# Performance work log

Measured on AMD Instinct MI355X. Metric: run time of the kernel, lower is better.

The kernel has to match this reference:

```python
import jax, jax.numpy as jnp
import numpy as np
import math

DIM = 1024
HEADS = 16
HEAD_DIM = DIM // HEADS
ROT = min(HEAD_DIM, 32)  # rotary_dim
B, S = 2, 1024


def setup_inputs() -> dict:
    key = jax.random.key(0)
    ks = jax.random.split(key, 32)
    lin = lambda k: jax.random.normal(k, (DIM, DIM), jnp.float32) * 0.02
    bias = lambda k: jax.random.normal(k, (DIM,), jnp.float32) * 0.01
    inp = {
        'real': jax.random.normal(ks[0], (B, S, DIM), jnp.float32),
        'imag': jax.random.normal(ks[1], (B, S, DIM), jnp.float32),
        'Wq_r': lin(ks[2]), 'bq_r': bias(ks[3]),
        'Wk_r': lin(ks[4]), 'bk_r': bias(ks[5]),
        'Wv_r': lin(ks[6]), 'bv_r': bias(ks[7]),
        'Wq_i': lin(ks[8]), 'bq_i': bias(ks[9]),
        'Wk_i': lin(ks[10]), 'bk_i': bias(ks[11]),
        'Wv_i': lin(ks[12]), 'bv_i': bias(ks[13]),
        'Wo_r': lin(ks[14]), 'bo_r': bias(ks[15]),
        'Wo_i': lin(ks[16]), 'bo_i': bias(ks[17]),
        'phase_shifts': jax.random.normal(ks[18], (HEADS, HEAD_DIM), jnp.float32) * 0.02,
        'ent': jnp.eye(HEADS, dtype=jnp.float32) + jax.random.normal(ks[19], (HEADS, HEADS), jnp.float32) * 0.01,
        'rot_freqs': (10000.0 ** (-jnp.arange(0, ROT, 2, dtype=jnp.float32) / ROT)),
        'strength': jnp.ones((1,), jnp.float32),
        'temp': jnp.ones((1,), jnp.float32),
    }
    return inp


def _fwd(real, imag, Wq_r, bq_r, Wk_r, bk_r, Wv_r, bv_r,
         Wq_i, bq_i, Wk_i, bk_i, Wv_i, bv_i,
         Wo_r, bo_r, Wo_i, bo_i,
         phase_shifts, ent, rot_freqs, strength, temp):
    b, s, _ = real.shape
    to_heads = lambda t: t.reshape(b, s, HEADS, HEAD_DIM).transpose(0, 2, 1, 3)  # bhsd
    lin = lambda x, W, bb: x @ W + bb

    q_r = to_heads(lin(real, Wq_r, bq_r))
    k_r = to_heads(lin(real, Wk_r, bk_r))
    v_r = to_heads(lin(real, Wv_r, bv_r))
    q_i = to_heads(lin(imag, Wq_i, bq_i))
    k_i = to_heads(lin(imag, Wk_i, bk_i))
    v_i = to_heads(lin(imag, Wv_i, bv_i))

    # rotary on first ROT dims (pairwise rotation)
    pos = jnp.arange(s, dtype=jnp.float32)
    emb = pos[:, None] * rot_freqs[None, :]           # [S, ROT/2]
    cos = jnp.cos(emb)[None, None]                    # [1,1,S,ROT/2]
    sin = jnp.sin(emb)[None, None]

    def rope(t):
        tr = t[..., :ROT].reshape(b, HEADS, s, ROT // 2, 2)
        r0 = tr[..., 0] * cos - tr[..., 1] * sin
        r1 = tr[..., 1] * cos + tr[..., 0] * sin
        rr = jnp.stack([r0, r1], axis=-1).reshape(b, HEADS, s, ROT)
        return jnp.concatenate([rr, t[..., ROT:]], axis=-1)

    q_r, k_r = rope(q_r), rope(k_r)
    q_i, k_i = rope(q_i), rope(k_i)

    # entanglement mixing across heads
    mix = lambda t: jnp.einsum('bhsd,hx->bxsd', t, ent)
    q_r, q_i, k_r, k_i = mix(q_r), mix(q_i), mix(k_r), mix(k_i)

    # per-head phase shift (complex rotation)
    pc = jnp.cos(phase_shifts)[None, :, None, :]      # [1,H,1,D]
    ps = jnp.sin(phase_shifts)[None, :, None, :]
    q_r, q_i = q_r * pc - q_i * ps, q_r * ps + q_i * pc
    k_r, k_i = k_r * pc - k_i * ps, k_r * ps + k_i * pc

    scale = 1.0 / math.sqrt(HEAD_DIM)
    attn_r = (jnp.einsum('bhqd,bhkd->bhqk', q_r, k_r) + jnp.einsum('bhqd,bhkd->bhqk', q_i, k_i)) * scale
    attn_i = (jnp.einsum('bhqd,bhkd->bhqk', q_i, k_r) - jnp.einsum('bhqd,bhkd->bhqk', q_r, k_i)) * scale
    attn_mag = jnp.sqrt(attn_r ** 2 + attn_i ** 2 + 1e-6)

    causal = jnp.triu(jnp.ones((s, s), dtype=bool), k=1)[None, None]
    attn_mag = jnp.where(causal, -jnp.inf, attn_mag)

    t = jnp.maximum(temp, 0.01)
    g = jax.nn.sigmoid(strength)
    attn = jax.nn.softmax(attn_mag * g / t, axis=-1)

    out_r = jnp.einsum('bhqk,bhkd->bhqd', attn, v_r).transpose(0, 2, 1, 3).reshape(b, s, DIM)
    out_i = jnp.einsum('bhqk,bhkd->bhqd', attn, v_i).transpose(0, 2, 1, 3).reshape(b, s, DIM)
    return lin(out_r, Wo_r, bo_r), lin(out_i, Wo_i, bo_i)


def reference(real, imag, Wq_r, bq_r, Wk_r, bk_r, Wv_r, bv_r,
              Wq_i, bq_i, Wk_i, bk_i, Wv_i, bv_i,
              Wo_r, bo_r, Wo_i, bo_i,
              phase_shifts, ent, rot_freqs, strength, temp):
    return _fwd(real, imag, Wq_r, bq_r, Wk_r, bk_r, Wv_r, bv_r,
                Wq_i, bq_i, Wk_i, bk_i, Wv_i, bv_i,
                Wo_r, bo_r, Wo_i, bo_i,
                phase_shifts, ent, rot_freqs, strength, temp)
```

## Files before the change

### kernel.cpp

```cpp
#include <hip/hip_runtime.h>
#include <stdint.h>

typedef unsigned short u16;
typedef __bf16 bf16x8 __attribute__((ext_vector_type(8)));
typedef float f32x4 __attribute__((ext_vector_type(4)));
typedef unsigned int u32x4 __attribute__((ext_vector_type(4)));

__device__ __forceinline__ u16 f2bf(float f) {
  uint32_t u = __float_as_uint(f);
  u += 0x7FFFu + ((u >> 16) & 1u);
  return (u16)(u >> 16);
}
__device__ __forceinline__ float bf2f(u16 h) {
  return __uint_as_float(((uint32_t)h) << 16);
}
__device__ __forceinline__ void gld16(const void* g, void* lds) {
  __builtin_amdgcn_global_load_lds(
      (const __attribute__((address_space(1))) uint32_t*)g,
      (__attribute__((address_space(3))) uint32_t*)lds, 16, 0, 0);
}
__device__ __forceinline__ f32x4 mfma16(u32x4 a, u32x4 b, f32x4 c) {
  return __builtin_amdgcn_mfma_f32_16x16x32_bf16(
      __builtin_bit_cast(bf16x8, a), __builtin_bit_cast(bf16x8, b), c, 0, 0, 0);
}

__global__ __launch_bounds__(256) void convx_kernel(const float* __restrict__ real,
                                                    const float* __restrict__ imag,
                                                    u16* __restrict__ Xr,
                                                    u16* __restrict__ Xi) {
  int u = blockIdx.x * 256 + threadIdx.x;
  int a = u >> 18;
  int r = u & 262143;
  int m = r >> 7, slot = r & 127;
  const float* src = (a ? imag : real) + (size_t)m * 1024 + slot * 8;
  int slot2 = (slot & ~7) | ((slot ^ m) & 7);
  u16* dst = (a ? Xi : Xr) + (size_t)m * 1024 + slot2 * 8;
  f32x4 v0 = *(const f32x4*)(src);
  f32x4 v1 = *(const f32x4*)(src + 4);
  union { u16 h[8]; u32x4 v; } o;
#pragma unroll
  for (int e = 0; e < 4; ++e) { o.h[e] = f2bf(v0[e]); o.h[4 + e] = f2bf(v1[e]); }
  *(u32x4*)dst = o.v;
}

__global__ __launch_bounds__(256) void convw_kernel(
    const float* __restrict__ w0, const float* __restrict__ w1,
    const float* __restrict__ w2, const float* __restrict__ w3,
    const float* __restrict__ w4, const float* __restrict__ w5,
    const float* __restrict__ w6, const float* __restrict__ w7,
    u16* __restrict__ WtAll) {
  __shared__ float Lt[64][65];
  int z = blockIdx.z;
  const float* W = (z == 0) ? w0 : (z == 1) ? w1 : (z == 2) ? w2 : (z == 3) ? w3
                 : (z == 4) ? w4 : (z == 5) ? w5 : (z == 6) ? w6 : w7;
  u16* Wt = WtAll + (size_t)z * (1024 * 1024);
  int tid = threadIdx.x;
  int n0 = blockIdx.x * 64, k0 = blockIdx.y * 64;
#pragma unroll
  for (int it = 0; it < 4; ++it) {
    int idx = it * 256 + tid;
    int kr = idx >> 4, nc = (idx & 15) * 4;
    f32x4 v = *(const f32x4*)(W + (size_t)(k0 + kr) * 1024 + n0 + nc);
#pragma unroll
    for (int e = 0; e < 4; ++e) Lt[kr][nc + e] = v[e];
  }
  __syncthreads();
#pragma unroll
  for (int it = 0; it < 2; ++it) {
    int idx = it * 256 + tid;
    int nr = idx >> 3, sl = idx & 7;
    union { u16 h[8]; u32x4 v; } o;
#pragma unroll
    for (int e = 0; e < 8; ++e) o.h[e] = f2bf(Lt[sl * 8 + e][nr]);
    int sl2 = sl ^ (nr & 7);
    *(u32x4*)(Wt + (size_t)(n0 + nr) * 1024 + k0 + sl2 * 8) = o.v;
  }
}

__device__ __forceinline__ void gemm128(const u16* __restrict__ A, const u16* __restrict__ W,
                                        const float* __restrict__ bias,
                                        u16* __restrict__ outB, float* __restrict__ outF) {
  __shared__ __align__(16) u16 As[128 * 64];
  __shared__ __align__(16) u16 Bs[128 * 64];
  int tid = threadIdx.x, l = tid & 63, w = tid >> 6;
  int lr = l & 15, lh = l >> 4;
  int m0 = blockIdx.y * 128, n0 = blockIdx.x * 128;
  int wr = w >> 1, wc = w & 1;
  f32x4 acc[4][4];
#pragma unroll
  for (int mi = 0; mi < 4; ++mi)
#pragma unroll
    for (int ni = 0; ni < 4; ++ni) acc[mi][ni] = f32x4{0.f, 0.f, 0.f, 0.f};

  for (int kt = 0; kt < 16; ++kt) {
#pragma unroll
    for (int c = 0; c < 4; ++c) {
      int chunk = c * 4 + w;
      int i = chunk * 64 + l;
      int row = i >> 3, off = i & 7;
      gld16(A + (size_t)(m0 + row) * 1024 + kt * 64 + off * 8, (char*)As + chunk * 1024);
      gld16(W + (size_t)(n0 + row) * 1024 + kt * 64 + off * 8, (char*)Bs + chunk * 1024);
    }
    __syncthreads();
#pragma unroll
    for (int kk = 0; kk < 2; ++kk) {
      u32x4 af[4], bf[4];
#pragma unroll
      for (int mi = 0; mi < 4; ++mi) {
        int row = wr * 64 + mi * 16 + lr;
        af[mi] = *(const u32x4*)((const char*)As + row * 128 +
                                 ((kk * 64 + lh * 16) ^ ((row & 7) << 4)));
      }
#pragma unroll
      for (int ni = 0; ni < 4; ++ni) {
        int row = wc * 64 + ni * 16 + lr;
        bf[ni] = *(const u32x4*)((const char*)Bs + row * 128 +
                                 ((kk * 64 + lh * 16) ^ ((row & 7) << 4)));
      }
#pragma unroll
      for (int mi = 0; mi < 4; ++mi)
#pragma unroll
        for (int ni = 0; ni < 4; ++ni)
          acc[mi][ni] = mfma16(af[mi], bf[ni], acc[mi][ni]);
    }
    __syncthreads();
  }
#pragma unroll
  for (int ni = 0; ni < 4; ++ni) {
    int col = n0 + wc * 64 + ni * 16 + lr;
    float bv = bias[col];
#pragma unroll
    for (int mi = 0; mi < 4; ++mi)
#pragma unroll
      for (int rr = 0; rr < 4; ++rr) {
        int row = m0 + wr * 64 + mi * 16 + 4 * lh + rr;
        float v = acc[mi][ni][rr] + bv;
        if (outF) outF[(size_t)row * 1024 + col] = v;
        else      outB[(size_t)row * 1024 + col] = f2bf(v);
      }
  }
}

__global__ __launch_bounds__(256) void gemm_proj_kernel(
    const u16* __restrict__ Xr, const u16* __restrict__ Xi, const u16* __restrict__ Wt,
    const float* b0, const float* b1, const float* b2,
    const float* b3, const float* b4, const float* b5,
    u16* __restrict__ qkv) {
  int z = blockIdx.z;
  const u16* A = (z < 3) ? Xr : Xi;
  const u16* W = Wt + (size_t)z * (1024 * 1024);
  const float* bias = (z == 0) ? b0 : (z == 1) ? b1 : (z == 2) ? b2
                    : (z == 3) ? b3 : (z == 4) ? b4 : b5;
  u16* out = qkv + (size_t)z * (2048 * 1024);
  gemm128(A, W, bias, out, nullptr);
}

__global__ __launch_bounds__(256) void gemm_out_kernel(
    const u16* __restrict__ O, const u16* __restrict__ Wt2,
    const float* br, const float* bi, float* __restrict__ dout) {
  int z = blockIdx.z;
  gemm128(O + (size_t)z * (2048 * 1024), Wt2 + (size_t)z * (1024 * 1024),
          z ? bi : br, nullptr, dout + (size_t)z * (2048 * 1024));
}

__global__ __launch_bounds__(256) void transform_kernel(
    const u16* __restrict__ qkv, const float* __restrict__ phase,
    const float* __restrict__ ent, const float* __restrict__ rotf,
    u16* __restrict__ Qr, u16* __restrict__ Qi, u16* __restrict__ Kr,
    u16* __restrict__ Ki, u16* __restrict__ Vr, u16* __restrict__ Vi) {
  __shared__ float Lqr[16][65], Lqi[16][65], Lkr[16][65], Lki[16][65];
  __shared__ float sent[256];
  int tid = threadIdx.x;
  int bs = blockIdx.x;
  int b = bs >> 10, s = bs & 1023;
  sent[tid] = ent[tid];
  const u16* qr_raw = qkv;
  const u16* kr_raw = qkv + (size_t)1 * 2048 * 1024;
  const u16* vr_raw = qkv + (size_t)2 * 2048 * 1024;
  const u16* qi_raw = qkv + (size_t)3 * 2048 * 1024;
  const u16* ki_raw = qkv + (size_t)4 * 2048 * 1024;
  const u16* vi_raw = qkv + (size_t)5 * 2048 * 1024;
  size_t rowoff = (size_t)bs * 1024;
#pragma unroll
  for (int it = 0; it < 2; ++it) {
    int u = it * 256 + tid;
    int hh = u >> 5, j = u & 31;
    int base = hh * 64 + 2 * j;
    uint32_t aqr = *(const uint32_t*)(qr_raw + rowoff + base);
    uint32_t aqi = *(const uint32_t*)(qi_raw + rowoff + base);
    uint32_t akr = *(const uint32_t*)(kr_raw + rowoff + base);
    uint32_t aki = *(const uint32_t*)(ki_raw + rowoff + base);
    float qr0 = bf2f((u16)aqr), qr1 = bf2f((u16)(aqr >> 16));
    float qi0 = bf2f((u16)aqi), qi1 = bf2f((u16)(aqi >> 16));
    float kr0 = bf2f((u16)akr), kr1 = bf2f((u16)(akr >> 16));
    float ki0 = bf2f((u16)aki), ki1 = bf2f((u16)(aki >> 16));
    if (j < 16) {
      float sn, cs;
      sincosf((float)s * rotf[j], &sn, &cs);
      float t0;
      t0 = qr0; qr0 = t0 * cs - qr1 * sn; qr1 = qr1 * cs + t0 * sn;
      t0 = qi0; qi0 = t0 * cs - qi1 * sn; qi1 = qi1 * cs + t0 * sn;
      t0 = kr0; kr0 = t0 * cs - kr1 * sn; kr1 = kr1 * cs + t0 * sn;
      t0 = ki0; ki0 = t0 * cs - ki1 * sn; ki1 = ki1 * cs + t0 * sn;
    }
    int d0 = 2 * j;
    Lqr[hh][d0] = qr0; Lqr[hh][d0 + 1] = qr1;
    Lqi[hh][d0] = qi0; Lqi[hh][d0 + 1] = qi1;
    Lkr[hh][d0] = kr0; Lkr[hh][d0 + 1] = kr1;
    Lki[hh][d0] = ki0; Lki[hh][d0 + 1] = ki1;
  }
  __syncthreads();
#pragma unroll
  for (int it = 0; it < 4; ++it) {
    int u = it * 256 + tid;
    int x = u >> 6, d = u & 63;
    float mqr = 0.f, mqi = 0.f, mkr = 0.f, mki = 0.f;
#pragma unroll
    for (int hh = 0; hh < 16; ++hh) {
      float e = sent[hh * 16 + x];
      mqr += Lqr[hh][d] * e; mqi += Lqi[hh][d] * e;
      mkr += Lkr[hh][d] * e; mki += Lki[hh][d] * e;
    }
    float ps_, pc_;
    sincosf(phase[x * 64 + d], &ps_, &pc_);
    float oqr = (mqr * pc_ - mqi * ps_) * 0.125f;
    float oqi = (mqr * ps_ + mqi * pc_) * 0.125f;
    float okr = mkr * pc_ - mki * ps_;
    float oki = mkr * ps_ + mki * pc_;
    size_t obase = ((size_t)(b * 16 + x) * 1024 + s) * 64;
    Qr[obase + d] = f2bf(oqr);
    Qi[obase + d] = f2bf(oqi);
    int dsw = (d & 7) | ((((d >> 3) ^ s) & 7) << 3);
    Kr[obase + dsw] = f2bf(okr);
    Ki[obase + dsw] = f2bf(oki);
  }
  {
    int u = tid;
    int comp = u >> 7, hh = (u >> 3) & 15, sl = u & 7;
    const u16* src = comp ? vi_raw : vr_raw;
    u16* dst = comp ? Vi : Vr;
    u32x4 vv = *(const u32x4*)(src + rowoff + hh * 64 + sl * 8);
    *(u32x4*)(dst + ((size_t)(b * 16 + hh) * 1024 + s) * 64 + sl * 8) = vv;
  }
}

__global__ __launch_bounds__(256) void transv_kernel(const u16* __restrict__ Vr,
                                                     const u16* __restrict__ Vi,
                                                     u16* __restrict__ VTr,
                                                     u16* __restrict__ VTi) {
  int bid = blockIdx.x;
  int comp = bid >> 9, bh = (bid >> 4) & 31, t = bid & 15;
  const u16* src = (comp ? Vi : Vr) + ((size_t)bh * 1024 + t * 64) * 64;
  u16* dst = (comp ? VTi : VTr) + (size_t)bh * 65536;
  __shared__ __align__(16) u16 Lt[64][72];
  int tid = threadIdx.x;
#pragma unroll
  for (int it = 0; it < 2; ++it) {
    int i = it * 256 + tid;
    int r = i >> 3, sl = i & 7;
    *(u32x4*)(&Lt[r][sl * 8]) = *(const u32x4*)(src + r * 64 + sl * 8);
  }
  __syncthreads();
#pragma unroll
  for (int it = 0; it < 2; ++it) {
    int i = it * 256 + tid;
    int d = i >> 3, sl = i & 7;
    union { u16 h[8]; u32x4 v; } o;
#pragma unroll
    for (int e = 0; e < 8; ++e) o.h[e] = Lt[sl * 8 + e][d];
    int sl2 = sl ^ (d & 7);
    *(u32x4*)(dst + (size_t)d * 1024 + t * 64 + sl2 * 8) = o.v;
  }
}

__global__ __launch_bounds__(256) void attn_kernel(
    const u16* __restrict__ Qr, const u16* __restrict__ Qi,
    const u16* __restrict__ Kr, const u16* __restrict__ Ki,
    const u16* __restrict__ VTr, const u16* __restrict__ VTi,
    const float* __restrict__ strength, const float* __restrict__ temp,
    u16* __restrict__ por0, u16* __restrict__ por1,
    u16* __restrict__ por2, u16* __restrict__ por3,
    u16* __restrict__ poi0, u16* __restrict__ poi1,
    u16* __restrict__ poi2, u16* __restrict__ poi3,
    float* __restrict__ Pm, float* __restrict__ Pl) {
  __shared__ __align__(16) u16 smem[20480];
  char* sb = (char*)smem;
  const int PO = 32768;
  int tid = threadIdx.x, l = tid & 63, w = tid >> 6;
  int lr = l & 15, lh = l >> 4;
  int id = blockIdx.x;
  int x = id & 7, j = id >> 3;
  int sp = j & 3, grp = j >> 2;
  int bh = x + 8 * (grp & 3);
  int qb = 15 - (grp >> 2);
  int b_ = bh >> 4; (void)b_;
  int q0 = qb * 64;
  int nt = qb + 1;
  int c = (nt + 3) >> 2;
  int t0 = sp * c, t1 = min(nt, t0 + c);
  u16* POr = (sp == 0) ? por0 : (sp == 1) ? por1 : (sp == 2) ? por2 : por3;
  u16* POi = (sp == 0) ? poi0 : (sp == 1) ? poi1 : (sp == 2) ? poi2 : poi3;

  f32x4 o_r[4], o_i[4];
#pragma unroll
  for (int n = 0; n < 4; ++n) { o_r[n] = f32x4{0,0,0,0}; o_i[n] = f32x4{0,0,0,0}; }
  float m_run[4], l_run[4];
#pragma unroll
  for (int rr = 0; rr < 4; ++rr) { m_run[rr] = -__builtin_inff(); l_run[rr] = 0.f; }

  if (t0 < t1) {
    float g = 1.f / (1.f + __expf(-strength[0]));
    float tt = fmaxf(temp[0], 0.01f);
    float gt = g / tt;

    size_t qbase = ((size_t)bh * 1024 + q0 + w * 16 + lr) * 64 + lh * 8;
    u32x4 qrF[2], qiF[2], nqrF[2];
#pragma unroll
    for (int kk = 0; kk < 2; ++kk) {
      qrF[kk] = *(const u32x4*)(Qr + qbase + kk * 32);
      qiF[kk] = *(const u32x4*)(Qi + qbase + kk * 32);
      nqrF[kk] = qrF[kk] ^ 0x80008000u;
    }

    for (int t = t0; t < t1; ++t) {
      if (w < 2) {
        const u16* Kp = (w ? Ki : Kr) + ((size_t)bh * 1024 + t * 64) * 64;
        char* dst = sb + (w ? 8192 : 0);
#pragma unroll
        for (int cc = 0; cc < 8; ++cc)
          gld16(Kp + cc * 512 + l * 8, dst + cc * 1024);
      } else {
        const u16* Vp = (w == 3 ? VTi : VTr) + (size_t)bh * 65536 + t * 64;
        char* dst = sb + (w == 3 ? 24576 : 16384);
#pragma unroll
        for (int cc = 0; cc < 8; ++cc) {
          int i = cc * 64 + l;
          int d = i >> 3, off = i & 7;
          gld16(Vp + (size_t)d * 1024 + off * 8, dst + cc * 1024);
        }
      }
      __syncthreads();

      f32x4 sr[4], si[4];
#pragma unroll
      for (int n = 0; n < 4; ++n) { sr[n] = f32x4{0,0,0,0}; si[n] = f32x4{0,0,0,0}; }
#pragma unroll
      for (int kk = 0; kk < 2; ++kk) {
#pragma unroll
        for (int n = 0; n < 4; ++n) {
          int kv = n * 16 + lr;
          int xoff = (kk * 64 + lh * 16) ^ ((kv & 7) << 4);
          u32x4 fkr = *(const u32x4*)(sb + kv * 128 + xoff);
          u32x4 fki = *(const u32x4*)(sb + 8192 + kv * 128 + xoff);
          sr[n] = mfma16(qrF[kk], fkr, sr[n]);
          sr[n] = mfma16(qiF[kk], fki, sr[n]);
          si[n] = mfma16(qiF[kk], fkr, si[n]);
          si[n] = mfma16(nqrF[kk], fki, si[n]);
        }
      }

      float pl[4][4], pm[4];
#pragma unroll
      for (int rr = 0; rr < 4; ++rr) pm[rr] = -__builtin_inff();
      bool diag = (t == qb);
#pragma unroll
      for (int n = 0; n < 4; ++n)
#pragma unroll
        for (int rr = 0; rr < 4; ++rr) {
          float a = sr[n][rr], cc = si[n][rr];
          float mag = sqrtf(a * a + cc * cc + 1e-6f) * gt;
          if (diag) {
            int colg = t * 64 + n * 16 + lr;
            int rowg = q0 + w * 16 + 4 * lh + rr;
            if (colg > rowg) mag = -__builtin_inff();
          }
          pl[n][rr] = mag;
          pm[rr] = fmaxf(pm[rr], mag);
        }
#pragma unroll
      for (int mk = 1; mk <= 8; mk <<= 1)
#pragma unroll
        for (int rr = 0; rr < 4; ++rr)
          pm[rr] = fmaxf(pm[rr], __shfl_xor(pm[rr], mk));
      float fr[4], rs[4];
#pragma unroll
      for (int rr = 0; rr < 4; ++rr) {
        float mnew = fmaxf(m_run[rr], pm[rr]);
        fr[rr] = __expf(m_run[rr] - mnew);
        m_run[rr] = mnew;
        rs[rr] = 0.f;
      }
#pragma unroll
      for (int n = 0; n < 4; ++n)
#pragma unroll
        for (int rr = 0; rr < 4; ++rr) {
          float p = __expf(pl[n][rr] - m_run[rr]);
          pl[n][rr] = p;
          rs[rr] += p;
        }
#pragma unroll
      for (int mk = 1; mk <= 8; mk <<= 1)
#pragma unroll
        for (int rr = 0; rr < 4; ++rr)
          rs[rr] += __shfl_xor(rs[rr], mk);
#pragma unroll
      for (int rr = 0; rr < 4; ++rr) l_run[rr] = l_run[rr] * fr[rr] + rs[rr];
#pragma unroll
      for (int n = 0; n < 4; ++n)
#pragma unroll
        for (int rr = 0; rr < 4; ++rr) { o_r[n][rr] *= fr[rr]; o_i[n][rr] *= fr[rr]; }

      char* pw = sb + PO + w * 2048;
#pragma unroll
      for (int n = 0; n < 4; ++n)
#pragma unroll
        for (int rr = 0; rr < 4; ++rr) {
          int row = 4 * lh + rr, col = n * 16 + lr;
          int by = row * 128 + ((col & 7) * 2) + ((((col >> 3) ^ row) & 7) << 4);
          *(u16*)(pw + by) = f2bf(pl[n][rr]);
        }
      u32x4 pf[2];
#pragma unroll
      for (int kk = 0; kk < 2; ++kk)
        pf[kk] = *(const u32x4*)(pw + lr * 128 + ((kk * 64 + lh * 16) ^ ((lr & 7) << 4)));
#pragma unroll
      for (int kk = 0; kk < 2; ++kk)
#pragma unroll
        for (int n = 0; n < 4; ++n) {
          int dl = n * 16 + lr;
          int xoff = (kk * 64 + lh * 16) ^ ((dl & 7) << 4);
          u32x4 fvr = *(const u32x4*)(sb + 16384 + dl * 128 + xoff);
          u32x4 fvi = *(const u32x4*)(sb + 24576 + dl * 128 + xoff);
          o_r[n] = mfma16(pf[kk], fvr, o_r[n]);
          o_i[n] = mfma16(pf[kk], fvi, o_i[n]);
        }
      __syncthreads();
    }
  }

  size_t pbase = ((size_t)bh * 1024 + q0 + w * 16 + 4 * lh) * 64;
#pragma unroll
  for (int n = 0; n < 4; ++n)
#pragma unroll
    for (int rr = 0; rr < 4; ++rr) {
      POr[pbase + rr * 64 + n * 16 + lr] = f2bf(o_r[n][rr]);
      POi[pbase + rr * 64 + n * 16 + lr] = f2bf(o_i[n][rr]);
    }
  if (lr == 0) {
    size_t mbase = (size_t)sp * 32768 + (size_t)bh * 1024 + q0 + w * 16 + 4 * lh;
#pragma unroll
    for (int rr = 0; rr < 4; ++rr) {
      Pm[mbase + rr] = m_run[rr];
      Pl[mbase + rr] = l_run[rr];
    }
  }
}

__global__ __launch_bounds__(256) void combine_kernel(
    const u16* __restrict__ por0, const u16* __restrict__ por1,
    const u16* __restrict__ por2, const u16* __restrict__ por3,
    const u16* __restrict__ poi0, const u16* __restrict__ poi1,
    const u16* __restrict__ poi2, const u16* __restrict__ poi3,
    const float* __restrict__ Pm, const float* __restrict__ Pl,
    u16* __restrict__ Or, u16* __restrict__ Oi) {
  int bid = blockIdx.x;
  int bh = bid >> 4, rg = bid & 15;
  int b = bh >> 4, h = bh & 15;
  int tid = threadIdx.x;
  int row = tid >> 2, q = tid & 3;
  int s = rg * 64 + row;
  size_t ro = (size_t)bh * 1024 + s;
  float m0 = Pm[ro], m1 = Pm[ro + 32768], m2 = Pm[ro + 65536], m3 = Pm[ro + 98304];
  float M = fmaxf(fmaxf(m0, m1), fmaxf(m2, m3));
  float e0 = __expf(m0 - M), e1 = __expf(m1 - M);
  float e2 = __expf(m2 - M), e3 = __expf(m3 - M);
  float lt = Pl[ro] * e0 + Pl[ro + 32768] * e1 + Pl[ro + 65536] * e2 + Pl[ro + 98304] * e3;
  float inv = 1.f / lt;
  float c0 = e0 * inv, c1 = e1 * inv, c2 = e2 * inv, c3 = e3 * inv;
  size_t obase = ro * 64;
#pragma unroll
  for (int g = 0; g < 2; ++g) {
    int d = q * 16 + g * 8;
    union { u16 h[8]; u32x4 v; } a0, a1, a2, a3;
    union { u16 h[8]; u32x4 v; } outr, outi;
    a0.v = *(const u32x4*)(por0 + obase + d);
    a1.v = *(const u32x4*)(por1 + obase + d);
    a2.v = *(const u32x4*)(por2 + obase + d);
    a3.v = *(const u32x4*)(por3 + obase + d);
#pragma unroll
    for (int e = 0; e < 8; ++e)
      outr.h[e] = f2bf(c0 * bf2f(a0.h[e]) + c1 * bf2f(a1.h[e]) +
                       c2 * bf2f(a2.h[e]) + c3 * bf2f(a3.h[e]));
    a0.v = *(const u32x4*)(poi0 + obase + d);
    a1.v = *(const u32x4*)(poi1 + obase + d);
    a2.v = *(const u32x4*)(poi2 + obase + d);
    a3.v = *(const u32x4*)(poi3 + obase + d);
#pragma unroll
    for (int e = 0; e < 8; ++e)
      outi.h[e] = f2bf(c0 * bf2f(a0.h[e]) + c1 * bf2f(a1.h[e]) +
                       c2 * bf2f(a2.h[e]) + c3 * bf2f(a3.h[e]));
    int slot2 = (d >> 3) ^ (s & 7);
    size_t oo = ((size_t)b * 1024 + s) * 1024 + h * 64 + slot2 * 8;
    *(u32x4*)(Or + oo) = outr.v;
    *(u32x4*)(Oi + oo) = outi.v;
  }
}

extern "C" void kernel_launch(void* const* d_in, const int* in_sizes, int n_in,
                              void* d_out, int out_size, void* d_ws, size_t ws_size,
                              hipStream_t stream) {
  (void)in_sizes; (void)n_in; (void)out_size; (void)ws_size;
  const float* real = (const float*)d_in[0];
  const float* imag = (const float*)d_in[1];
  const float* bq_r = (const float*)d_in[3];
  const float* bk_r = (const float*)d_in[5];
  const float* bv_r = (const float*)d_in[7];
  const float* bq_i = (const float*)d_in[9];
  const float* bk_i = (const float*)d_in[11];
  const float* bv_i = (const float*)d_in[13];
  const float* bo_r = (const float*)d_in[15];
  const float* bo_i = (const float*)d_in[17];
  const float* phase = (const float*)d_in[18];
  const float* ent = (const float*)d_in[19];
  const float* rotf = (const float*)d_in[20];
  const float* strength = (const float*)d_in[21];
  const float* temp = (const float*)d_in[22];

  u16* ws = (u16*)d_ws;
  const size_t M1 = 1024 * 1024, M2 = 2048 * 1024;
  u16* Xr  = ws;
  u16* Xi  = Xr + M2;
  u16* Wt  = Xi + M2;
  u16* qkv = Wt + 8 * M1;
  u16* Qr  = qkv + 6 * M2;
  u16* Qi  = Qr + M2;
  u16* Kr  = Qi + M2;
  u16* Ki  = Kr + M2;
  u16* Vr  = Ki + M2;
  u16* Vi  = Vr + M2;
  u16* VTr = Vi + M2;
  u16* VTi = VTr + M2;
  u16* Or  = VTi + M2;
  u16* Oi  = Or + M2;
  u16* por0 = qkv;
  u16* por1 = qkv + M2;
  u16* por2 = qkv + 2 * M2;
  u16* por3 = qkv + 3 * M2;
  u16* poi0 = qkv + 4 * M2;
  u16* poi1 = qkv + 5 * M2;
  u16* poi2 = Vr;
  u16* poi3 = Vi;
  float* Pm = (float*)Xr;
  float* Pl = Pm + 131072;

  convx_kernel<<<2048, 256, 0, stream>>>(real, imag, Xr, Xi);
  convw_kernel<<<dim3(16, 16, 8), 256, 0, stream>>>(
      (const float*)d_in[2],  (const float*)d_in[4],  (const float*)d_in[6],
      (const float*)d_in[8],  (const float*)d_in[10], (const float*)d_in[12],
      (const float*)d_in[14], (const float*)d_in[16], Wt);
  gemm_proj_kernel<<<dim3(8, 16, 6), 256, 0, stream>>>(Xr, Xi, Wt, bq_r, bk_r, bv_r,
                                                       bq_i, bk_i, bv_i, qkv);
  transform_kernel<<<2048, 256, 0, stream>>>(qkv, phase, ent, rotf, Qr, Qi, Kr, Ki, Vr, Vi);
  transv_kernel<<<1024, 256, 0, stream>>>(Vr, Vi, VTr, VTi);
  attn_kernel<<<2048, 256, 0, stream>>>(Qr, Qi, Kr, Ki, VTr, VTi, strength, temp,
                                        por0, por1, por2, por3,
                                        poi0, poi1, poi2, poi3, Pm, Pl);
  combine_kernel<<<512, 256, 0, stream>>>(por0, por1, por2, por3,
                                          poi0, poi1, poi2, poi3, Pm, Pl, Or, Oi);
  gemm_out_kernel<<<dim3(8, 16, 2), 256, 0, stream>>>(Or, Wt + 6 * M1, bo_r, bo_i,
                                                      (float*)d_out);
}
```

Baseline: 157.5 us.

## Precompute trig tables, rebalance attention splits, defer softmax rescale, trim combine

A new tables kernel precomputes the rotary and phase sin/cos values, so the transform kernel reads them instead of calling sincosf per element. The attention grid moves from 2048 blocks with a uniform four-way split to 1280 blocks with a fixed 4-tile chunk per split, so short query blocks use fewer splits and no block is empty. The attention kernel also skips the running-max rescale when the max grows by at most 8, uses a raw v_sqrt instruction, and simplifies the causal-mask index math. The combine kernel reads only the splits that exist for each row group. The table lives in the Oi buffer, which is safe only if Oi is not written before the transform kernel consumes it.

```diff
diff --git a/kernel.cpp b/kernel.cpp
--- a/kernel.cpp
+++ b/kernel.cpp
@@ -14,6 +14,9 @@
 __device__ __forceinline__ float bf2f(u16 h) {
   return __uint_as_float(((uint32_t)h) << 16);
 }
+__device__ __forceinline__ float fsqrt(float x) {
+  float r; asm("v_sqrt_f32 %0, %1" : "=v"(r) : "v"(x)); return r;
+}
 __device__ __forceinline__ void gld16(const void* g, void* lds) {
   __builtin_amdgcn_global_load_lds(
       (const __attribute__((address_space(1))) uint32_t*)g,
@@ -22,6 +25,25 @@
 __device__ __forceinline__ f32x4 mfma16(u32x4 a, u32x4 b, f32x4 c) {
   return __builtin_amdgcn_mfma_f32_16x16x32_bf16(
       __builtin_bit_cast(bf16x8, a), __builtin_bit_cast(bf16x8, b), c, 0, 0, 0);
+}
+
+__global__ __launch_bounds__(256) void tables_kernel(const float* __restrict__ rotf,
+                                                     const float* __restrict__ phase,
+                                                     float* __restrict__ T) {
+  int id = blockIdx.x * 256 + threadIdx.x;
+  if (id < 16384) {
+    int s = id >> 4, jj = id & 15;
+    float sn, cs;
+    sincosf((float)s * rotf[jj], &sn, &cs);
+    T[id] = cs;
+    T[16384 + id] = sn;
+  } else if (id < 16384 + 1024) {
+    int p = id - 16384;
+    float sn, cs;
+    sincosf(phase[p], &sn, &cs);
+    T[32768 + p] = cs;
+    T[33792 + p] = sn;
+  }
 }
 
 __global__ __launch_bounds__(256) void convx_kernel(const float* __restrict__ real,
@@ -164,8 +186,8 @@
 }
 
 __global__ __launch_bounds__(256) void transform_kernel(
-    const u16* __restrict__ qkv, const float* __restrict__ phase,
-    const float* __restrict__ ent, const float* __restrict__ rotf,
+    const u16* __restrict__ qkv, const float* __restrict__ ent,
+    const float* __restrict__ T,
     u16* __restrict__ Qr, u16* __restrict__ Qi, u16* __restrict__ Kr,
     u16* __restrict__ Ki, u16* __restrict__ Vr, u16* __restrict__ Vi) {
   __shared__ float Lqr[16][65], Lqi[16][65], Lkr[16][65], Lki[16][65];
@@ -195,8 +217,8 @@
     float kr0 = bf2f((u16)akr), kr1 = bf2f((u16)(akr >> 16));
     float ki0 = bf2f((u16)aki), ki1 = bf2f((u16)(aki >> 16));
     if (j < 16) {
-      float sn, cs;
-      sincosf((float)s * rotf[j], &sn, &cs);
+      float cs = T[s * 16 + j];
+      float sn = T[16384 + s * 16 + j];
       float t0;
       t0 = qr0; qr0 = t0 * cs - qr1 * sn; qr1 = qr1 * cs + t0 * sn;
       t0 = qi0; qi0 = t0 * cs - qi1 * sn; qi1 = qi1 * cs + t0 * sn;
@@ -221,8 +243,8 @@
       mqr += Lqr[hh][d] * e; mqi += Lqi[hh][d] * e;
       mkr += Lkr[hh][d] * e; mki += Lki[hh][d] * e;
     }
-    float ps_, pc_;
-    sincosf(phase[x * 64 + d], &ps_, &pc_);
+    float pc_ = T[32768 + x * 64 + d];
+    float ps_ = T[33792 + x * 64 + d];
     float oqr = (mqr * pc_ - mqi * ps_) * 0.125f;
     float oqi = (mqr * ps_ + mqi * pc_) * 0.125f;
     float okr = mkr * pc_ - mki * ps_;
@@ -290,17 +312,31 @@
   int lr = l & 15, lh = l >> 4;
   int id = blockIdx.x;
   int x = id & 7, j = id >> 3;
-  int sp = j & 3, grp = j >> 2;
-  int bh = x + 8 * (grp & 3);
-  int qb = 15 - (grp >> 2);
-  int b_ = bh >> 4; (void)b_;
+  int bh = x + 8 * (j & 3);
+  int cc = j >> 2;
+  int qb, sp;
+  if (cc < 16)      { qb = 15 - (cc >> 2); sp = cc & 3; }
+  else if (cc < 28) { int r = cc - 16; int q3 = r / 3; qb = 11 - q3; sp = r - 3 * q3; }
+  else if (cc < 36) { int r = cc - 28; qb = 7 - (r >> 1); sp = r & 1; }
+  else              { qb = 39 - cc; sp = 0; }
   int q0 = qb * 64;
-  int nt = qb + 1;
-  int c = (nt + 3) >> 2;
-  int t0 = sp * c, t1 = min(nt, t0 + c);
+  int t0 = sp * 4, t1 = min(qb + 1, t0 + 4);
+  int b = bh >> 4; (void)b;
   u16* POr = (sp == 0) ? por0 : (sp == 1) ? por1 : (sp == 2) ? por2 : por3;
   u16* POi = (sp == 0) ? poi0 : (sp == 1) ? poi1 : (sp == 2) ? poi2 : poi3;
 
+  float g = 1.f / (1.f + __expf(-strength[0]));
+  float tt = fmaxf(temp[0], 0.01f);
+  float gt = g / tt;
+
+  size_t qbase = ((size_t)bh * 1024 + q0 + w * 16 + lr) * 64 + lh * 8;
+  u32x4 qrF[2], qiF[2], nqrF[2];
+#pragma unroll
+  for (int kk = 0; kk < 2; ++kk) {
+    qrF[kk] = *(const u32x4*)(Qr + qbase + kk * 32);
+    qiF[kk] = *(const u32x4*)(Qi + qbase + kk * 32);
+    nqrF[kk] = qrF[kk] ^ 0x80008000u;
+  }
   f32x4 o_r[4], o_i[4];
 #pragma unroll
   for (int n = 0; n < 4; ++n) { o_r[n] = f32x4{0,0,0,0}; o_i[n] = f32x4{0,0,0,0}; }
@@ -308,134 +344,130 @@
 #pragma unroll
   for (int rr = 0; rr < 4; ++rr) { m_run[rr] = -__builtin_inff(); l_run[rr] = 0.f; }
 
-  if (t0 < t1) {
-    float g = 1.f / (1.f + __expf(-strength[0]));
-    float tt = fmaxf(temp[0], 0.01f);
-    float gt = g / tt;
-
-    size_t qbase = ((size_t)bh * 1024 + q0 + w * 16 + lr) * 64 + lh * 8;
-    u32x4 qrF[2], qiF[2], nqrF[2];
+  const u16* gK = ((w == 1) ? Ki : Kr) + ((size_t)bh * 1024 + t0 * 64) * 64 + l * 8;
+  char* ldK = sb + (w == 1 ? 8192 : 0);
+  const u16* gV = ((w == 3) ? VTi : VTr) + (size_t)bh * 65536 + t0 * 64 +
+                  (l >> 3) * 1024 + (l & 7) * 8;
+  char* ldV = sb + (w == 3 ? 24576 : 16384);
+
+  for (int t = t0; t < t1; ++t) {
+    if (w < 2) {
+#pragma unroll
+      for (int c = 0; c < 8; ++c) gld16(gK + c * 512, ldK + c * 1024);
+      gK += 4096;
+    } else {
+#pragma unroll
+      for (int c = 0; c < 8; ++c) gld16(gV + c * 8192, ldV + c * 1024);
+      gV += 64;
+    }
+    __syncthreads();
+
+    f32x4 sr[4], si[4];
+#pragma unroll
+    for (int n = 0; n < 4; ++n) { sr[n] = f32x4{0,0,0,0}; si[n] = f32x4{0,0,0,0}; }
 #pragma unroll
     for (int kk = 0; kk < 2; ++kk) {
-      qrF[kk] = *(const u32x4*)(Qr + qbase + kk * 32);
-      qiF[kk] = *(const u32x4*)(Qi + qbase + kk * 32);
-      nqrF[kk] = qrF[kk] ^ 0x80008000u;
-    }
-
-    for (int t = t0; t < t1; ++t) {
-      if (w < 2) {
-        const u16* Kp = (w ? Ki : Kr) + ((size_t)bh * 1024 + t * 64) * 64;
-        char* dst = sb + (w ? 8192 : 0);
-#pragma unroll
-        for (int cc = 0; cc < 8; ++cc)
-          gld16(Kp + cc * 512 + l * 8, dst + cc * 1024);
-      } else {
-        const u16* Vp = (w == 3 ? VTi : VTr) + (size_t)bh * 65536 + t * 64;
-        char* dst = sb + (w == 3 ? 24576 : 16384);
-#pragma unroll
-        for (int cc = 0; cc < 8; ++cc) {
-          int i = cc * 64 + l;
-          int d = i >> 3, off = i & 7;
-          gld16(Vp + (size_t)d * 1024 + off * 8, dst + cc * 1024);
+#pragma unroll
+      for (int n = 0; n < 4; ++n) {
+        int kv = n * 16 + lr;
+        int xoff = (kk * 64 + lh * 16) ^ ((kv & 7) << 4);
+        u32x4 fkr = *(const u32x4*)(sb + kv * 128 + xoff);
+        u32x4 fki = *(const u32x4*)(sb + 8192 + kv * 128 + xoff);
+        sr[n] = mfma16(qrF[kk], fkr, sr[n]);
+        sr[n] = mfma16(qiF[kk], fki, sr[n]);
+        si[n] = mfma16(qiF[kk], fkr, si[n]);
+        si[n] = mfma16(nqrF[kk], fki, si[n]);
+      }
+    }
+
+    float pl[4][4], pm[4];
+#pragma unroll
+    for (int rr = 0; rr < 4; ++rr) pm[rr] = -__builtin_inff();
+    bool diag = (t == qb);
+#pragma unroll
+    for (int n = 0; n < 4; ++n)
+#pragma unroll
+      for (int rr = 0; rr < 4; ++rr) {
+        float a = sr[n][rr], ci = si[n][rr];
+        float mag = fsqrt(a * a + ci * ci + 1e-6f) * gt;
+        if (diag) {
+          if (n * 16 + lr > w * 16 + 4 * lh + rr) mag = -__builtin_inff();
         }
-      }
-      __syncthreads();
-
-      f32x4 sr[4], si[4];
-#pragma unroll
-      for (int n = 0; n < 4; ++n) { sr[n] = f32x4{0,0,0,0}; si[n] = f32x4{0,0,0,0}; }
-#pragma unroll
-      for (int kk = 0; kk < 2; ++kk) {
-#pragma unroll
-        for (int n = 0; n < 4; ++n) {
-          int kv = n * 16 + lr;
-          int xoff = (kk * 64 + lh * 16) ^ ((kv & 7) << 4);
-          u32x4 fkr = *(const u32x4*)(sb + kv * 128 + xoff);
-          u32x4 fki = *(const u32x4*)(sb + 8192 + kv * 128 + xoff);
-          sr[n] = mfma16(qrF[kk], fkr, sr[n]);
-          sr[n] = mfma16(qiF[kk], fki, sr[n]);
-          si[n] = mfma16(qiF[kk], fkr, si[n]);
-          si[n] = mfma16(nqrF[kk], fki, si[n]);
-        }
-      }
-
-      float pl[4][4], pm[4];
-#pragma unroll
-      for (int rr = 0; rr < 4; ++rr) pm[rr] = -__builtin_inff();
-      bool diag = (t == qb);
-#pragma unroll
-      for (int n = 0; n < 4; ++n)
-#pragma unroll
-        for (int rr = 0; rr < 4; ++rr) {
-          float a = sr[n][rr], cc = si[n][rr];
-          float mag = sqrtf(a * a + cc * cc + 1e-6f) * gt;
-          if (diag) {
-            int colg = t * 64 + n * 16 + lr;
-            int rowg = q0 + w * 16 + 4 * lh + rr;
-            if (colg > rowg) mag = -__builtin_inff();
-          }
-          pl[n][rr] = mag;
-          pm[rr] = fmaxf(pm[rr], mag);
-        }
-#pragma unroll
-      for (int mk = 1; mk <= 8; mk <<= 1)
-#pragma unroll
-        for (int rr = 0; rr < 4; ++rr)
-          pm[rr] = fmaxf(pm[rr], __shfl_xor(pm[rr], mk));
-      float fr[4], rs[4];
+        pl[n][rr] = mag;
+        pm[rr] = fmaxf(pm[rr], mag);
+      }
+#pragma unroll
+    for (int mk = 1; mk <= 8; mk <<= 1)
+#pragma unroll
+      for (int rr = 0; rr < 4; ++rr)
+        pm[rr] = fmaxf(pm[rr], __shfl_xor(pm[rr], mk));
+
+    bool defer = true;
+#pragma unroll
+    for (int rr = 0; rr < 4; ++rr) defer = defer && (pm[rr] - m_run[rr] <= 8.f);
+    bool noresc = __all(defer ? 1 : 0);
+    float fr[4];
+    if (!noresc) {
 #pragma unroll
       for (int rr = 0; rr < 4; ++rr) {
         float mnew = fmaxf(m_run[rr], pm[rr]);
         fr[rr] = __expf(m_run[rr] - mnew);
         m_run[rr] = mnew;
-        rs[rr] = 0.f;
-      }
+      }
+    }
+    float rs[4];
+#pragma unroll
+    for (int rr = 0; rr < 4; ++rr) rs[rr] = 0.f;
+#pragma unroll
+    for (int n = 0; n < 4; ++n)
+#pragma unroll
+      for (int rr = 0; rr < 4; ++rr) {
+        float p = __expf(pl[n][rr] - m_run[rr]);
+        pl[n][rr] = p;
+        rs[rr] += p;
+      }
+#pragma unroll
+    for (int mk = 1; mk <= 8; mk <<= 1)
+#pragma unroll
+      for (int rr = 0; rr < 4; ++rr)
+        rs[rr] += __shfl_xor(rs[rr], mk);
+    if (!noresc) {
+#pragma unroll
+      for (int rr = 0; rr < 4; ++rr) l_run[rr] = l_run[rr] * fr[rr] + rs[rr];
 #pragma unroll
       for (int n = 0; n < 4; ++n)
 #pragma unroll
-        for (int rr = 0; rr < 4; ++rr) {
-          float p = __expf(pl[n][rr] - m_run[rr]);
-          pl[n][rr] = p;
-          rs[rr] += p;
-        }
-#pragma unroll
-      for (int mk = 1; mk <= 8; mk <<= 1)
-#pragma unroll
-        for (int rr = 0; rr < 4; ++rr)
-          rs[rr] += __shfl_xor(rs[rr], mk);
-#pragma unroll
-      for (int rr = 0; rr < 4; ++rr) l_run[rr] = l_run[rr] * fr[rr] + rs[rr];
-#pragma unroll
-      for (int n = 0; n < 4; ++n)
-#pragma unroll
         for (int rr = 0; rr < 4; ++rr) { o_r[n][rr] *= fr[rr]; o_i[n][rr] *= fr[rr]; }
-
-      char* pw = sb + PO + w * 2048;
-#pragma unroll
-      for (int n = 0; n < 4; ++n)
-#pragma unroll
-        for (int rr = 0; rr < 4; ++rr) {
-          int row = 4 * lh + rr, col = n * 16 + lr;
-          int by = row * 128 + ((col & 7) * 2) + ((((col >> 3) ^ row) & 7) << 4);
-          *(u16*)(pw + by) = f2bf(pl[n][rr]);
-        }
-      u32x4 pf[2];
-#pragma unroll
-      for (int kk = 0; kk < 2; ++kk)
-        pf[kk] = *(const u32x4*)(pw + lr * 128 + ((kk * 64 + lh * 16) ^ ((lr & 7) << 4)));
-#pragma unroll
-      for (int kk = 0; kk < 2; ++kk)
-#pragma unroll
-        for (int n = 0; n < 4; ++n) {
-          int dl = n * 16 + lr;
-          int xoff = (kk * 64 + lh * 16) ^ ((dl & 7) << 4);
-          u32x4 fvr = *(const u32x4*)(sb + 16384 + dl * 128 + xoff);
-          u32x4 fvi = *(const u32x4*)(sb + 24576 + dl * 128 + xoff);
-          o_r[n] = mfma16(pf[kk], fvr, o_r[n]);
-          o_i[n] = mfma16(pf[kk], fvi, o_i[n]);
-        }
-      __syncthreads();
-    }
+    } else {
+#pragma unroll
+      for (int rr = 0; rr < 4; ++rr) l_run[rr] += rs[rr];
+    }
+
+    char* pw = sb + PO + w * 2048;
+#pragma unroll
+    for (int n = 0; n < 4; ++n)
+#pragma unroll
+      for (int rr = 0; rr < 4; ++rr) {
+        int row = 4 * lh + rr, col = n * 16 + lr;
+        int by = row * 128 + ((col & 7) * 2) + ((((col >> 3) ^ row) & 7) << 4);
+        *(u16*)(pw + by) = f2bf(pl[n][rr]);
+      }
+    u32x4 pf[2];
+#pragma unroll
+    for (int kk = 0; kk < 2; ++kk)
+      pf[kk] = *(const u32x4*)(pw + lr * 128 + ((kk * 64 + lh * 16) ^ ((lr & 7) << 4)));
+#pragma unroll
+    for (int kk = 0; kk < 2; ++kk)
+#pragma unroll
+      for (int n = 0; n < 4; ++n) {
+        int dl = n * 16 + lr;
+        int xoff = (kk * 64 + lh * 16) ^ ((dl & 7) << 4);
+        u32x4 fvr = *(const u32x4*)(sb + 16384 + dl * 128 + xoff);
+        u32x4 fvi = *(const u32x4*)(sb + 24576 + dl * 128 + xoff);
+        o_r[n] = mfma16(pf[kk], fvr, o_r[n]);
+        o_i[n] = mfma16(pf[kk], fvi, o_i[n]);
+      }
+    __syncthreads();
   }
 
   size_t pbase = ((size_t)bh * 1024 + q0 + w * 16 + 4 * lh) * 64;
@@ -466,39 +498,55 @@
   int bid = blockIdx.x;
   int bh = bid >> 4, rg = bid & 15;
   int b = bh >> 4, h = bh & 15;
+  int ns = (rg >> 2) + 1;
   int tid = threadIdx.x;
   int row = tid >> 2, q = tid & 3;
   int s = rg * 64 + row;
   size_t ro = (size_t)bh * 1024 + s;
-  float m0 = Pm[ro], m1 = Pm[ro + 32768], m2 = Pm[ro + 65536], m3 = Pm[ro + 98304];
-  float M = fmaxf(fmaxf(m0, m1), fmaxf(m2, m3));
-  float e0 = __expf(m0 - M), e1 = __expf(m1 - M);
-  float e2 = __expf(m2 - M), e3 = __expf(m3 - M);
-  float lt = Pl[ro] * e0 + Pl[ro + 32768] * e1 + Pl[ro + 65536] * e2 + Pl[ro + 98304] * e3;
+  const u16* PR[4] = {por0, por1, por2, por3};
+  const u16* PI[4] = {poi0, poi1, poi2, poi3};
+  float msp[4], lsp[4], csw[4];
+  float M = -__builtin_inff();
+#pragma unroll
+  for (int sp = 0; sp < 4; ++sp) {
+    if (sp < ns) {
+      msp[sp] = Pm[ro + (size_t)sp * 32768];
+      lsp[sp] = Pl[ro + (size_t)sp * 32768];
+      M = fmaxf(M, msp[sp]);
+    }
+  }
+  float lt = 0.f;
+#pragma unroll
+  for (int sp = 0; sp < 4; ++sp) {
+    if (sp < ns) { csw[sp] = __expf(msp[sp] - M); lt += lsp[sp] * csw[sp]; }
+    else csw[sp] = 0.f;
+  }
   float inv = 1.f / lt;
-  float c0 = e0 * inv, c1 = e1 * inv, c2 = e2 * inv, c3 = e3 * inv;
+#pragma unroll
+  for (int sp = 0; sp < 4; ++sp) csw[sp] *= inv;
   size_t obase = ro * 64;
 #pragma unroll
   for (int g = 0; g < 2; ++g) {
     int d = q * 16 + g * 8;
-    union { u16 h[8]; u32x4 v; } a0, a1, a2, a3;
+    float accr[8], acci[8];
+#pragma unroll
+    for (int e = 0; e < 8; ++e) { accr[e] = 0.f; acci[e] = 0.f; }
+#pragma unroll
+    for (int sp = 0; sp < 4; ++sp) {
+      if (sp < ns) {
+        union { u16 h[8]; u32x4 v; } ar, ai;
+        ar.v = *(const u32x4*)(PR[sp] + obase + d);
+        ai.v = *(const u32x4*)(PI[sp] + obase + d);
+#pragma unroll
+        for (int e = 0; e < 8; ++e) {
+          accr[e] += csw[sp] * bf2f(ar.h[e]);
+          acci[e] += csw[sp] * bf2f(ai.h[e]);
+        }
+      }
+    }
     union { u16 h[8]; u32x4 v; } outr, outi;
-    a0.v = *(const u32x4*)(por0 + obase + d);
-    a1.v = *(const u32x4*)(por1 + obase + d);
-    a2.v = *(const u32x4*)(por2 + obase + d);
-    a3.v = *(const u32x4*)(por3 + obase + d);
-#pragma unroll
-    for (int e = 0; e < 8; ++e)
-      outr.h[e] = f2bf(c0 * bf2f(a0.h[e]) + c1 * bf2f(a1.h[e]) +
-                       c2 * bf2f(a2.h[e]) + c3 * bf2f(a3.h[e]));
-    a0.v = *(const u32x4*)(poi0 + obase + d);
-    a1.v = *(const u32x4*)(poi1 + obase + d);
-    a2.v = *(const u32x4*)(poi2 + obase + d);
-    a3.v = *(const u32x4*)(poi3 + obase + d);
-#pragma unroll
-    for (int e = 0; e < 8; ++e)
-      outi.h[e] = f2bf(c0 * bf2f(a0.h[e]) + c1 * bf2f(a1.h[e]) +
-                       c2 * bf2f(a2.h[e]) + c3 * bf2f(a3.h[e]));
+#pragma unroll
+    for (int e = 0; e < 8; ++e) { outr.h[e] = f2bf(accr[e]); outi.h[e] = f2bf(acci[e]); }
     int slot2 = (d >> 3) ^ (s & 7);
     size_t oo = ((size_t)b * 1024 + s) * 1024 + h * 64 + slot2 * 8;
     *(u32x4*)(Or + oo) = outr.v;
@@ -552,7 +600,9 @@
   u16* poi3 = Vi;
   float* Pm = (float*)Xr;
   float* Pl = Pm + 131072;
-
+  float* TBL = (float*)Oi;
+
+  tables_kernel<<<68, 256, 0, stream>>>(rotf, phase, TBL);
   convx_kernel<<<2048, 256, 0, stream>>>(real, imag, Xr, Xi);
   convw_kernel<<<dim3(16, 16, 8), 256, 0, stream>>>(
       (const float*)d_in[2],  (const float*)d_in[4],  (const float*)d_in[6],
@@ -560,9 +610,9 @@
       (const float*)d_in[14], (const float*)d_in[16], Wt);
   gemm_proj_kernel<<<dim3(8, 16, 6), 256, 0, stream>>>(Xr, Xi, Wt, bq_r, bk_r, bv_r,
                                                        bq_i, bk_i, bv_i, qkv);
-  transform_kernel<<<2048, 256, 0, stream>>>(qkv, phase, ent, rotf, Qr, Qi, Kr, Ki, Vr, Vi);
+  transform_kernel<<<2048, 256, 0, stream>>>(qkv, ent, TBL, Qr, Qi, Kr, Ki, Vr, Vi);
   transv_kernel<<<1024, 256, 0, stream>>>(Vr, Vi, VTr, VTi);
-  attn_kernel<<<2048, 256, 0, stream>>>(Qr, Qi, Kr, Ki, VTr, VTi, strength, temp,
+  attn_kernel<<<1280, 256, 0, stream>>>(Qr, Qi, Kr, Ki, VTr, VTi, strength, temp,
                                         por0, por1, por2, por3,
                                         poi0, poi1, poi2, poi3, Pm, Pl);
   combine_kernel<<<512, 256, 0, stream>>>(por0, por1, por2, por3,
```

Result: no change. 157.1 us (-0.2%).
